# Optimization experiments

Hardware: AMD Instinct MI355X
Metric: run time of the kernel (lower is better)

The kernel has to match this reference:

```python
import jax, jax.numpy as jnp
import numpy as np

KROT = 8
DIM = 4096
GROUP = 128
N = 16384  # tokens (batch*seq)


def setup_inputs() -> dict:
    key = jax.random.key(0)
    k1, k2, k3 = jax.random.split(key, 3)
    x = jax.random.normal(k1, (N, DIM), dtype=jnp.float16)
    theta = (jax.random.normal(k2, (KROT, DIM // 2)) * 0.5).astype(jnp.float16)
    # pairs: per rotation layer, a permutation of [0, GROUP) tiled across groups
    # (matches torch.randperm(group_size).repeat(num_groups) in the module).
    rng = np.random.default_rng(0)
    single = np.stack([rng.permutation(GROUP) for _ in range(KROT)]).astype(np.int32)  # (KROT, GROUP)
    pairs = jnp.asarray(np.tile(single, (1, DIM // GROUP)))  # (KROT, DIM)
    channel_scales = jax.random.uniform(k3, (1, DIM), minval=0.5, maxval=1.5).astype(jnp.float16)
    return {"x": x, "pairs": pairs, "theta": theta,
            "channel_scales": channel_scales, "group_size": GROUP}


def reference(x, pairs, theta, channel_scales, group_size):
    """Pairwise Givens rotations + per-channel scaling.

    For each rotation layer k, channels are grouped into blocks of
    `group_size`; consecutive entries (pairs[k, 2i], pairs[k, 2i+1]) within a
    group define a rotated channel pair with angle theta[k, i].
    """
    krot, dim = pairs.shape
    # global channel index = group offset + within-group index from `pairs`
    offs = (jnp.arange(dim) // group_size) * group_size            # (dim,)
    gidx = pairs + offs[None, :]                                   # (krot, dim)
    a_idx = gidx[:, 0::2]                                          # (krot, dim//2)
    b_idx = gidx[:, 1::2]                                          # (krot, dim//2)

    for k in range(krot):  # krot is a small fixed constant (8)
        t = theta[k].astype(jnp.float32)
        c = jnp.cos(t).astype(x.dtype)                             # (dim//2,)
        s = jnp.sin(t).astype(x.dtype)
        xa = x[:, a_idx[k]]                                        # (N, dim//2)
        xb = x[:, b_idx[k]]
        x = x.at[:, a_idx[k]].set(c * xa - s * xb)
        x = x.at[:, b_idx[k]].set(s * xa + c * xb)
    return x * channel_scales
```

## Files before the change

kernel.cpp:

```cpp
#include <hip/hip_runtime.h>
#include <hip/hip_fp16.h>


typedef unsigned int uint32;

#define DIM    4096
#define GROUP  128
#define KROT   8
#define NGROUP 32

__device__ __forceinline__ float bf16_to_f(unsigned short u) {
    union { uint32 i; float f; } v; v.i = ((uint32)u) << 16; return v.f;
}
__device__ __forceinline__ unsigned short f_to_bf16(float f) {
    union { float f; uint32 i; } v; v.f = f;
    uint32 x = v.i;
    return (unsigned short)((x + 0x7fffu + ((x >> 16) & 1u)) >> 16);
}
__device__ __forceinline__ float fp16_to_f(unsigned short u) {
    __half h = __ushort_as_half(u); return __half2float(h);
}
__device__ __forceinline__ unsigned short f_to_fp16(float f) {
    return __half_as_ushort(__float2half_rn(f));
}

__global__ __launch_bounds__(256) void detect_dtype(const uint32* __restrict__ scw,
                                                    int* __restrict__ flag) {
    __shared__ int cbf[256], cfp16[256];
    int b = 0, h = 0;
    for (int i = threadIdx.x; i < 2048; i += 256) {
        uint32 lo = scw[i] & 0xffffu;
        b += (lo >= 0x3F00u && lo <= 0x3FC0u);
        h += (lo >= 0x3800u && lo <= 0x3E00u);
    }
    cbf[threadIdx.x] = b; cfp16[threadIdx.x] = h;
    __syncthreads();
    for (int s = 128; s > 0; s >>= 1) {
        if (threadIdx.x < s) { cbf[threadIdx.x] += cbf[threadIdx.x + s];
                               cfp16[threadIdx.x] += cfp16[threadIdx.x + s]; }
        __syncthreads();
    }
    if (threadIdx.x == 0)
        *flag = (cbf[0] > 1024) ? 1 : ((cfp16[0] > 1024) ? 2 : 0);
}

__global__ __launch_bounds__(256) void rotate_direct(
    const void* __restrict__ Xv,
    const int*  __restrict__ pairs,
    const void* __restrict__ thetav,
    const void* __restrict__ scalesv,
    void* __restrict__ Outv,
    const int* __restrict__ flagp, int defflag)
{
    __shared__ float tile[64][GROUP + 2];
    __shared__ float scl[GROUP];
    const int g    = blockIdx.x;
    const int row0 = blockIdx.y * 64;
    const int tid  = threadIdx.x;
    const int dt   = flagp ? *flagp : defflag;

    if (tid < GROUP) {
        int c = g * GROUP + tid;
        scl[tid] = (dt == 1) ? bf16_to_f(((const unsigned short*)scalesv)[c])
                 : (dt == 2) ? fp16_to_f(((const unsigned short*)scalesv)[c])
                 : ((const float*)scalesv)[c];
    }

    const int p   = tid & 63;
    const int wr0 = (tid >> 6) * 16;
    int Ak[KROT], Bk[KROT]; float ck[KROT], sk[KROT];
    #pragma unroll
    for (int k = 0; k < KROT; ++k) {
        Ak[k] = pairs[k * DIM + g * GROUP + 2 * p];
        Bk[k] = pairs[k * DIM + g * GROUP + 2 * p + 1];
        int ti = k * (DIM / 2) + g * (GROUP / 2) + p;
        float th = (dt == 1) ? bf16_to_f(((const unsigned short*)thetav)[ti])
                 : (dt == 2) ? fp16_to_f(((const unsigned short*)thetav)[ti])
                 : ((const float*)thetav)[ti];
        ck[k] = __builtin_cosf(th);
        sk[k] = __builtin_sinf(th);
    }

    if (dt == 0) {
        const float4* X4 = (const float4*)Xv;
        for (int i = tid; i < 64 * 32; i += 256) {
            int r = i >> 5, c4 = i & 31;
            float4 v = X4[(size_t)(row0 + r) * (DIM / 4) + g * (GROUP / 4) + c4];
            tile[r][c4 * 4 + 0] = v.x; tile[r][c4 * 4 + 1] = v.y;
            tile[r][c4 * 4 + 2] = v.z; tile[r][c4 * 4 + 3] = v.w;
        }
    } else {
        const uint4* X4 = (const uint4*)Xv;
        for (int i = tid; i < 64 * 16; i += 256) {
            int r = i >> 4, c8 = i & 15;
            uint4 w = X4[(size_t)(row0 + r) * (DIM / 8) + g * (GROUP / 8) + c8];
            uint32 ws[4] = { w.x, w.y, w.z, w.w };
            #pragma unroll
            for (int h2 = 0; h2 < 4; ++h2) {
                unsigned short lo = (unsigned short)(ws[h2] & 0xffffu);
                unsigned short hi = (unsigned short)(ws[h2] >> 16);
                tile[r][c8 * 8 + 2 * h2]     = (dt == 1) ? bf16_to_f(lo) : fp16_to_f(lo);
                tile[r][c8 * 8 + 2 * h2 + 1] = (dt == 1) ? bf16_to_f(hi) : fp16_to_f(hi);
            }
        }
    }
    __syncthreads();

    #pragma unroll
    for (int k = 0; k < KROT; ++k) {
        #pragma unroll
        for (int rr = 0; rr < 16; ++rr) {
            int r = wr0 + rr;
            float xa = tile[r][Ak[k]], xb = tile[r][Bk[k]];
            tile[r][Ak[k]] = ck[k] * xa - sk[k] * xb;
            tile[r][Bk[k]] = sk[k] * xa + ck[k] * xb;
        }
    }
    __syncthreads();

    if (dt == 0) {
        float4* O4 = (float4*)Outv;
        for (int i = tid; i < 64 * 32; i += 256) {
            int r = i >> 5, c4 = i & 31;
            float4 v;
            v.x = tile[r][c4 * 4 + 0] * scl[c4 * 4 + 0];
            v.y = tile[r][c4 * 4 + 1] * scl[c4 * 4 + 1];
            v.z = tile[r][c4 * 4 + 2] * scl[c4 * 4 + 2];
            v.w = tile[r][c4 * 4 + 3] * scl[c4 * 4 + 3];
            O4[(size_t)(row0 + r) * (DIM / 4) + g * (GROUP / 4) + c4] = v;
        }
    } else {
        uint4* O4 = (uint4*)Outv;
        for (int i = tid; i < 64 * 16; i += 256) {
            int r = i >> 4, c8 = i & 15;
            uint32 ws[4];
            #pragma unroll
            for (int h2 = 0; h2 < 4; ++h2) {
                float lo = tile[r][c8 * 8 + 2 * h2]     * scl[c8 * 8 + 2 * h2];
                float hi = tile[r][c8 * 8 + 2 * h2 + 1] * scl[c8 * 8 + 2 * h2 + 1];
                unsigned short ulo = (dt == 1) ? f_to_bf16(lo) : f_to_fp16(lo);
                unsigned short uhi = (dt == 1) ? f_to_bf16(hi) : f_to_fp16(hi);
                ws[h2] = (uint32)ulo | ((uint32)uhi << 16);
            }
            uint4 w; w.x = ws[0]; w.y = ws[1]; w.z = ws[2]; w.w = ws[3];
            O4[(size_t)(row0 + r) * (DIM / 8) + g * (GROUP / 8) + c8] = w;
        }
    }
}

extern "C" void kernel_launch(void* const* d_in, const int* in_sizes, int n_in,
                              void* d_out, int out_size, void* d_ws, size_t ws_size,
                              hipStream_t stream) {
    const void* x      = d_in[0];
    const int*  pairs  = (const int*)d_in[1];
    const void* theta  = d_in[2];
    const void* scales = d_in[3];

    const int N = in_sizes[0] / DIM;
    const int nrowtiles = N / 64;

    int* flag = nullptr;
    if (d_ws != nullptr && ws_size >= sizeof(int)) {
        flag = (int*)d_ws;
        detect_dtype<<<1, 256, 0, stream>>>((const uint32*)scales, flag);
    }
    rotate_direct<<<dim3(NGROUP, nrowtiles), 256, 0, stream>>>(
        x, pairs, theta, scales, d_out, flag, 0);
}
```

Before: 517.6 us.

## Remap rotation loop so lanes own rows and broadcast pair params via readlane

Reassigns work in the rotation phase so each lane handles one tile row while each wave iterates over 16 pairs, broadcasting pair indices and cos/sin with readlane. Row padding is changed to an odd stride so lanes accessing the same column in different rows hit distinct LDS banks, removing conflicts caused by random pair columns. Requires a block barrier after each rotation layer since different waves now touch the same rows, adding synchronization cost.

```diff
diff --git a/kernel.cpp b/kernel.cpp
--- a/kernel.cpp
+++ b/kernel.cpp
@@ -8,6 +8,7 @@
 #define GROUP  128
 #define KROT   8
 #define NGROUP 32
+#define TPAD   (GROUP + 1)
 
 __device__ __forceinline__ float bf16_to_f(unsigned short u) {
     union { uint32 i; float f; } v; v.i = ((uint32)u) << 16; return v.f;
@@ -22,6 +23,9 @@
 }
 __device__ __forceinline__ unsigned short f_to_fp16(float f) {
     return __half_as_ushort(__float2half_rn(f));
+}
+__device__ __forceinline__ float bcast_f(float x, int lane) {
+    return __uint_as_float(__builtin_amdgcn_readlane(__float_as_uint(x), lane));
 }
 
 __global__ __launch_bounds__(256) void detect_dtype(const uint32* __restrict__ scw,
@@ -52,12 +56,15 @@
     void* __restrict__ Outv,
     const int* __restrict__ flagp, int defflag)
 {
-    __shared__ float tile[64][GROUP + 2];
+    __shared__ float tile[64][TPAD];
     __shared__ float scl[GROUP];
     const int g    = blockIdx.x;
     const int row0 = blockIdx.y * 64;
     const int tid  = threadIdx.x;
     const int dt   = flagp ? *flagp : defflag;
+    const int l    = tid & 63;
+    const int w    = tid >> 6;
+    const int pmine = w * 16 + (l & 15);
 
     if (tid < GROUP) {
         int c = g * GROUP + tid;
@@ -66,19 +73,17 @@
                  : ((const float*)scalesv)[c];
     }
 
-    const int p   = tid & 63;
-    const int wr0 = (tid >> 6) * 16;
-    int Ak[KROT], Bk[KROT]; float ck[KROT], sk[KROT];
+    int A[KROT], B[KROT]; float C[KROT], S[KROT];
     #pragma unroll
     for (int k = 0; k < KROT; ++k) {
-        Ak[k] = pairs[k * DIM + g * GROUP + 2 * p];
-        Bk[k] = pairs[k * DIM + g * GROUP + 2 * p + 1];
-        int ti = k * (DIM / 2) + g * (GROUP / 2) + p;
+        A[k] = pairs[k * DIM + g * GROUP + 2 * pmine];
+        B[k] = pairs[k * DIM + g * GROUP + 2 * pmine + 1];
+        int ti = k * (DIM / 2) + g * (GROUP / 2) + pmine;
         float th = (dt == 1) ? bf16_to_f(((const unsigned short*)thetav)[ti])
                  : (dt == 2) ? fp16_to_f(((const unsigned short*)thetav)[ti])
                  : ((const float*)thetav)[ti];
-        ck[k] = __builtin_cosf(th);
-        sk[k] = __builtin_sinf(th);
+        C[k] = __builtin_cosf(th);
+        S[k] = __builtin_sinf(th);
     }
 
     if (dt == 0) {
@@ -93,8 +98,8 @@
         const uint4* X4 = (const uint4*)Xv;
         for (int i = tid; i < 64 * 16; i += 256) {
             int r = i >> 4, c8 = i & 15;
-            uint4 w = X4[(size_t)(row0 + r) * (DIM / 8) + g * (GROUP / 8) + c8];
-            uint32 ws[4] = { w.x, w.y, w.z, w.w };
+            uint4 wv = X4[(size_t)(row0 + r) * (DIM / 8) + g * (GROUP / 8) + c8];
+            uint32 ws[4] = { wv.x, wv.y, wv.z, wv.w };
             #pragma unroll
             for (int h2 = 0; h2 < 4; ++h2) {
                 unsigned short lo = (unsigned short)(ws[h2] & 0xffffu);
@@ -109,14 +114,17 @@
     #pragma unroll
     for (int k = 0; k < KROT; ++k) {
         #pragma unroll
-        for (int rr = 0; rr < 16; ++rr) {
-            int r = wr0 + rr;
-            float xa = tile[r][Ak[k]], xb = tile[r][Bk[k]];
-            tile[r][Ak[k]] = ck[k] * xa - sk[k] * xb;
-            tile[r][Bk[k]] = sk[k] * xa + ck[k] * xb;
+        for (int pp = 0; pp < 16; ++pp) {
+            int   a = __builtin_amdgcn_readlane(A[k], pp);
+            int   b = __builtin_amdgcn_readlane(B[k], pp);
+            float c = bcast_f(C[k], pp);
+            float s = bcast_f(S[k], pp);
+            float xa = tile[l][a], xb = tile[l][b];
+            tile[l][a] = c * xa - s * xb;
+            tile[l][b] = s * xa + c * xb;
         }
+        __syncthreads();
     }
-    __syncthreads();
 
     if (dt == 0) {
         float4* O4 = (float4*)Outv;
@@ -142,8 +150,8 @@
                 unsigned short uhi = (dt == 1) ? f_to_bf16(hi) : f_to_fp16(hi);
                 ws[h2] = (uint32)ulo | ((uint32)uhi << 16);
             }
-            uint4 w; w.x = ws[0]; w.y = ws[1]; w.z = ws[2]; w.w = ws[3];
-            O4[(size_t)(row0 + r) * (DIM / 8) + g * (GROUP / 8) + c8] = w;
+            uint4 wv; wv.x = ws[0]; wv.y = ws[1]; wv.z = ws[2]; wv.w = ws[3];
+            O4[(size_t)(row0 + r) * (DIM / 8) + g * (GROUP / 8) + c8] = wv;
         }
     }
 }
```

New measurement: 481.3 us. 1.08x faster.
